# Kernel optimization log

Hardware: AMD Instinct MI355X
Metric: run time of the kernel (lower is better)

## Reference

```python
import jax, jax.numpy as jnp
import numpy as np

B, D = 8192, 512
NUM_CLASSES, K = 90, 8


def setup_inputs() -> dict:
    key = jax.random.key(0)
    kx, kc, kl = jax.random.split(key, 3)
    x = jax.random.normal(kx, (B, D), dtype=jnp.float32)
    centers = jax.random.normal(kc, (NUM_CLASSES, K, D), dtype=jnp.float32)
    labels = jax.random.randint(kl, (B,), 0, NUM_CLASSES, dtype=jnp.int64)
    return {"x": x, "centers": centers, "labels": labels}


def reference(x, centers, labels):
    # Gather per-sample class centers: [B, K, D]
    c = centers[labels]
    # inner_dsts[b, k] = 1 + <x_b, center_{label_b, k}>
    d = 1.0 + jnp.einsum('bd,bkd->bk', x, c)
    # weights are detached (stop-gradient) normalized inner distances
    w = jax.lax.stop_gradient(d)
    w = w / jnp.sum(w, axis=-1, keepdims=True)
    # per-sample weighted sum, then mean over batch (original sums then /batch_size)
    return jnp.mean(jnp.sum(w * d, axis=-1))
```

## Files before the change

kernel.cpp:

```cpp
#include <hip/hip_runtime.h>

#define BATCH      8192
#define D_DIM      512
#define NUM_CLS    90
#define K_CENTERS  8

typedef float v4f __attribute__((ext_vector_type(4)));

__global__ __launch_bounds__(256) void center_loss_main(
    const float* __restrict__ x,
    const float* __restrict__ centers,
    const int*   __restrict__ labels,
    double*      __restrict__ partials)
{
    const int wave = threadIdx.x >> 6;
    const int lane = threadIdx.x & 63;
    const int k    = lane & 7;
    const int sub  = lane >> 3;

    const int b = blockIdx.x * 4 + wave;

    __shared__ double s_r[4];

    double r = 0.0;
    if (b < BATCH) {
        const int label = labels[b];
        const v4f* xr = (const v4f*)(x + (size_t)b * D_DIM) + sub;
        const v4f* cr = (const v4f*)(centers + ((size_t)label * K_CENTERS + k) * D_DIM) + sub;

        float acc = 0.0f;
#pragma unroll
        for (int i = 0; i < 16; ++i) {
            v4f xv = __builtin_nontemporal_load(xr + i * 8);
            v4f cv = cr[i * 8];
            acc = fmaf(xv.x, cv.x, acc);
            acc = fmaf(xv.y, cv.y, acc);
            acc = fmaf(xv.z, cv.z, acc);
            acc = fmaf(xv.w, cv.w, acc);
        }
        acc += __shfl_xor(acc, 8);
        acc += __shfl_xor(acc, 16);
        acc += __shfl_xor(acc, 32);

        const float dk = 1.0f + acc;
        float s1 = dk;
        float s2 = dk * dk;
        s1 += __shfl_xor(s1, 1);  s2 += __shfl_xor(s2, 1);
        s1 += __shfl_xor(s1, 2);  s2 += __shfl_xor(s2, 2);
        s1 += __shfl_xor(s1, 4);  s2 += __shfl_xor(s2, 4);

        r = (double)(s2 / s1);
    }

    if (lane == 0) s_r[wave] = r;
    __syncthreads();
    if (threadIdx.x == 0) {
        partials[blockIdx.x] = s_r[0] + s_r[1] + s_r[2] + s_r[3];
    }
}

__global__ __launch_bounds__(256) void center_loss_reduce(
    const double* __restrict__ partials,
    float*        __restrict__ out,
    int n)
{
    double s = 0.0;
    for (int i = threadIdx.x; i < n; i += 256) s += partials[i];

    s += __shfl_xor(s, 1);
    s += __shfl_xor(s, 2);
    s += __shfl_xor(s, 4);
    s += __shfl_xor(s, 8);
    s += __shfl_xor(s, 16);
    s += __shfl_xor(s, 32);

    __shared__ double sm[4];
    const int wave = threadIdx.x >> 6;
    const int lane = threadIdx.x & 63;
    if (lane == 0) sm[wave] = s;
    __syncthreads();
    if (threadIdx.x == 0) {
        double t = sm[0] + sm[1] + sm[2] + sm[3];
        out[0] = (float)(t / (double)BATCH);
    }
}

extern "C" void kernel_launch(void* const* d_in, const int* in_sizes, int n_in,
                              void* d_out, int out_size, void* d_ws, size_t ws_size,
                              hipStream_t stream) {
    const float* x       = (const float*)d_in[0];
    const float* centers = (const float*)d_in[1];
    const int*   labels  = (const int*)d_in[2];
    float*  out      = (float*)d_out;
    double* partials = (double*)d_ws;

    const int nblocks = BATCH / 4;
    center_loss_main<<<nblocks, 256, 0, stream>>>(x, centers, labels, partials);
    center_loss_reduce<<<1, 256, 0, stream>>>(partials, out, nblocks);
}
```

Baseline: 27.54 us.

## Fuse final reduction into main kernel via atomics and last-block completion

Replaces the two-kernel scheme (per-block partials plus a single-block reduce) with one fused kernel. Each block now processes two samples per wave, halving the grid, and adds its partial into one of 8 padded double slots with atomics. The last block to arrive, detected with an atomic counter, sums the slots and writes the output. This removes the second kernel launch and the serial reduction tail, but adds a memset launch, atomic contention, and a nondeterministic order of double summation.

```diff
diff --git a/kernel.cpp b/kernel.cpp
--- a/kernel.cpp
+++ b/kernel.cpp
@@ -7,23 +7,29 @@
 
 typedef float v4f __attribute__((ext_vector_type(4)));
 
-__global__ __launch_bounds__(256) void center_loss_main(
+#define N_SLOTS 8
+
+__global__ __launch_bounds__(256) void center_loss_fused(
     const float* __restrict__ x,
     const float* __restrict__ centers,
     const int*   __restrict__ labels,
-    double*      __restrict__ partials)
+    double*      __restrict__ slots,
+    unsigned*    __restrict__ cnt,
+    float*       __restrict__ out)
 {
     const int wave = threadIdx.x >> 6;
     const int lane = threadIdx.x & 63;
     const int k    = lane & 7;
     const int sub  = lane >> 3;
 
-    const int b = blockIdx.x * 4 + wave;
+    const int g = blockIdx.x * 4 + wave;
 
     __shared__ double s_r[4];
 
     double r = 0.0;
-    if (b < BATCH) {
+#pragma unroll
+    for (int s = 0; s < 2; ++s) {
+        const int b = g + s * 4096;
         const int label = labels[b];
         const v4f* xr = (const v4f*)(x + (size_t)b * D_DIM) + sub;
         const v4f* cr = (const v4f*)(centers + ((size_t)label * K_CENTERS + k) * D_DIM) + sub;
@@ -49,39 +55,28 @@
         s1 += __shfl_xor(s1, 2);  s2 += __shfl_xor(s2, 2);
         s1 += __shfl_xor(s1, 4);  s2 += __shfl_xor(s2, 4);
 
-        r = (double)(s2 / s1);
+        r += (double)(s2 / s1);
     }
 
     if (lane == 0) s_r[wave] = r;
     __syncthreads();
+
     if (threadIdx.x == 0) {
-        partials[blockIdx.x] = s_r[0] + s_r[1] + s_r[2] + s_r[3];
-    }
-}
-
-__global__ __launch_bounds__(256) void center_loss_reduce(
-    const double* __restrict__ partials,
-    float*        __restrict__ out,
-    int n)
-{
-    double s = 0.0;
-    for (int i = threadIdx.x; i < n; i += 256) s += partials[i];
-
-    s += __shfl_xor(s, 1);
-    s += __shfl_xor(s, 2);
-    s += __shfl_xor(s, 4);
-    s += __shfl_xor(s, 8);
-    s += __shfl_xor(s, 16);
-    s += __shfl_xor(s, 32);
-
-    __shared__ double sm[4];
-    const int wave = threadIdx.x >> 6;
-    const int lane = threadIdx.x & 63;
-    if (lane == 0) sm[wave] = s;
-    __syncthreads();
-    if (threadIdx.x == 0) {
-        double t = sm[0] + sm[1] + sm[2] + sm[3];
-        out[0] = (float)(t / (double)BATCH);
+        const double p = s_r[0] + s_r[1] + s_r[2] + s_r[3];
+        double* slot = slots + (size_t)(blockIdx.x & (N_SLOTS - 1)) * 16;
+        __hip_atomic_fetch_add(slot, p, __ATOMIC_RELAXED, __HIP_MEMORY_SCOPE_AGENT);
+        __threadfence();
+        const unsigned old = __hip_atomic_fetch_add(cnt, 1u, __ATOMIC_ACQ_REL,
+                                                    __HIP_MEMORY_SCOPE_AGENT);
+        if (old == gridDim.x - 1) {
+            double t = 0.0;
+#pragma unroll
+            for (int i = 0; i < N_SLOTS; ++i) {
+                t += __hip_atomic_load(slots + (size_t)i * 16, __ATOMIC_RELAXED,
+                                       __HIP_MEMORY_SCOPE_AGENT);
+            }
+            out[0] = (float)(t / (double)BATCH);
+        }
     }
 }
 
@@ -91,10 +86,12 @@
     const float* x       = (const float*)d_in[0];
     const float* centers = (const float*)d_in[1];
     const int*   labels  = (const int*)d_in[2];
-    float*  out      = (float*)d_out;
-    double* partials = (double*)d_ws;
+    float*    out   = (float*)d_out;
+    double*   slots = (double*)d_ws;
+    unsigned* cnt   = (unsigned*)((char*)d_ws + 1024);
 
-    const int nblocks = BATCH / 4;
-    center_loss_main<<<nblocks, 256, 0, stream>>>(x, centers, labels, partials);
-    center_loss_reduce<<<1, 256, 0, stream>>>(partials, out, nblocks);
+    hipMemsetAsync(d_ws, 0, 2048, stream);
+
+    const int nblocks = BATCH / 8;
+    center_loss_fused<<<nblocks, 256, 0, stream>>>(x, centers, labels, slots, cnt, out);
 }
```

Measured after the change: 56.84 us. 106% more time.
